# Performance work log

Hardware: AMD Instinct MI355X
Metric: run time of the kernel (lower is better)

## Reference

```python
import jax, jax.numpy as jnp
import numpy as np

EPS = 1e-7  # K.epsilon()
SIZE_IN, IN_CAPS, KSIZE, STRIDE, CAPS, ROUTINGS = 14, 32, 3, 2, 32, 3
SIZE_OUT = (SIZE_IN - KSIZE) // STRIDE + 1  # 6
P = SIZE_OUT * SIZE_OUT          # 36 parent positions
C = KSIZE * KSIZE * IN_CAPS      # 288 child capsules per parent


def _child_parent_map():
    idx = []
    valid = range(0, SIZE_IN - KSIZE + 1, STRIDE)
    for row in valid:
        for col in valid:
            for kr in range(KSIZE):
                start = (row + kr) * SIZE_IN + col
                idx.extend(range(start, start + KSIZE))
    return np.asarray(idx, dtype=np.int32).reshape(P, KSIZE * KSIZE)

CPM = _child_parent_map()  # [P, K^2] static gather indices


def _em_routing(in_act, votes, beta_a, beta_v):
    # in_act: [B,P,C,1,1]; votes: [B,P,C,O,16]
    O = CAPS
    rr = jnp.full(votes.shape[:4] + (1,), 1.0 / O, dtype=votes.dtype)
    bv = beta_v.reshape(1, 1, 1, O, 1)
    ba = beta_a.reshape(1, 1, 1, O)
    out_act = means = None
    for i in range(ROUTINGS):
        lambd = 0.01 * (1.0 - 0.95 ** i)
        # ---- M step ----
        rr_scaled = rr * in_act                                   # [B,P,C,O,1]
        rr_sum = jnp.sum(rr_scaled, axis=2, keepdims=True)        # [B,P,1,O,1]
        means = jnp.sum(rr_scaled * votes, axis=2, keepdims=True) / (rr_sum + EPS)  # [B,P,1,O,16]
        std = jnp.sqrt(jnp.sum(rr_scaled * jnp.square(votes - means), axis=2, keepdims=True) / (rr_sum + EPS))
        costs = bv + jnp.log(std + EPS) * rr_sum                  # [B,P,1,O,16]
        out_act = jax.nn.sigmoid(lambd * (ba - jnp.sum(costs, axis=-1)))[..., None]  # [B,P,1,O,1]
        # ---- E step ----
        if i < ROUTINGS - 1:
            prob_exp = -jnp.sum(jnp.square(votes - means) / (2.0 * jnp.square(std) + EPS), axis=-1, keepdims=True)
            prob_main = -jnp.sum(jnp.log(std + EPS), axis=-1, keepdims=True)
            zz = jnp.log(out_act + EPS) + prob_main + prob_exp   # [B,P,C,O,1]
            rr = jax.nn.softmax(zz, axis=3)
    return out_act, means


def setup_inputs() -> dict:
    key = jax.random.key(0)
    k1, k2, k3, k4, k5 = jax.random.split(key, 5)
    B = 8
    return {
        "in_act": jax.random.uniform(k1, (B, SIZE_IN, SIZE_IN, IN_CAPS, 1), dtype=jnp.float32),
        "in_pose": jax.random.normal(k2, (B, SIZE_IN, SIZE_IN, IN_CAPS, 4, 4), dtype=jnp.float32),
        "W": jax.random.normal(k3, (1, 1, C, CAPS, 4, 4), dtype=jnp.float32) * 0.1,
        "beta_a": jax.random.normal(k4, (CAPS,), dtype=jnp.float32),
        "beta_v": jax.random.normal(k5, (CAPS,), dtype=jnp.float32),
    }


def reference(in_act, in_pose, W, beta_a, beta_v):
    B = in_act.shape[0]
    act = in_act.reshape(B, SIZE_IN * SIZE_IN, IN_CAPS)
    pose = in_pose.reshape(B, SIZE_IN * SIZE_IN, IN_CAPS, 4, 4)
    # gather children for each parent window -> [B,P,C,...]
    act_g = act[:, CPM].reshape(B, P, C, 1, 1)
    pose_g = pose[:, CPM].reshape(B, P, C, 4, 4)
    # votes[b,p,c,o,i,j] = sum_k pose_g[b,p,c,i,k] * W[c,o,k,j]
    votes = jnp.einsum('bpcik,cokj->bpcoij', pose_g, W.reshape(C, CAPS, 4, 4))
    votes = votes.reshape(B, P, C, CAPS, 16)
    out_act, out_pose = _em_routing(act_g, votes, beta_a, beta_v)
    out_act = out_act.reshape(B, SIZE_OUT, SIZE_OUT, CAPS, 1)
    out_pose = out_pose.reshape(B, SIZE_OUT, SIZE_OUT, CAPS, 4, 4)
    return out_act, out_pose
```

## Files before the change

kernel.cpp:

```cpp
#include <hip/hip_runtime.h>
#include <math.h>

#define EPS 1e-7f

constexpr int SIZE_IN = 14;
constexpr int P_  = 36;
constexpr int Cc  = 288;
constexpr int O_  = 32;
constexpr int G_  = 4;
constexpr int CG  = Cc / G_;
constexpr int NTG = CG / 8;
constexpr int THREADS = 256;
constexpr int NBP = 8 * P_;
constexpr int MIVS = 36;

template<int CTRL>
__device__ __forceinline__ float dppf(float x) {
    int xi = __builtin_bit_cast(int, x);
    return __builtin_bit_cast(float,
        __builtin_amdgcn_update_dpp(xi, xi, CTRL, 0xf, 0xf, true));
}
__device__ __forceinline__ float swz16(float x) {
    return __builtin_bit_cast(float,
        __builtin_amdgcn_ds_swizzle(__builtin_bit_cast(int, x), 0x401F));
}
__device__ __forceinline__ float red32_max(float x) {
    x = fmaxf(x, dppf<0xB1>(x));
    x = fmaxf(x, dppf<0x4E>(x));
    x = fmaxf(x, dppf<0x141>(x));
    x = fmaxf(x, dppf<0x140>(x));
    x = fmaxf(x, swz16(x));
    return x;
}
__device__ __forceinline__ float red32_sum(float x) {
    x += dppf<0xB1>(x);
    x += dppf<0x4E>(x);
    x += dppf<0x141>(x);
    x += dppf<0x140>(x);
    x += swz16(x);
    return x;
}
__device__ __forceinline__ float red16_sum(float x) {
    x += dppf<0xB1>(x);
    x += dppf<0x4E>(x);
    x += dppf<0x141>(x);
    x += dppf<0x140>(x);
    return x;
}

#define F4_TO_ARR(dst, off, f4) \
    dst[(off)+0] = (f4).x; dst[(off)+1] = (f4).y; dst[(off)+2] = (f4).z; dst[(off)+3] = (f4).w;


struct __align__(16) PassMem {
    float pose[CG * 16];
    float act[CG];
    float red[4][O_][33];
    float miv[O_][33];
};

template<bool HASE>
__global__ __launch_bounds__(THREADS, 1) void caps_pass(
    const float* __restrict__ in_act, const float* __restrict__ in_pose,
    const float* __restrict__ W, const float* __restrict__ MIV,
    float* __restrict__ Pout)
{
    __shared__ PassMem sm;
    const int blk = blockIdx.x;
    const int bp = blk >> 2, g = blk & 3;
    const int b  = bp / P_,  p = bp % P_;
    const int tid = threadIdx.x;
    const int row0 = (p / 6) * 2, col0 = (p % 6) * 2;

    for (int f = tid; f < CG * 4; f += THREADS) {
        const int fq = g * (CG * 4) + f;
        const int qw = fq >> 7, r = fq & 127;
        const int pix = (row0 + qw / 3) * SIZE_IN + (col0 + qw % 3);
        reinterpret_cast<float4*>(sm.pose)[f] =
            reinterpret_cast<const float4*>(in_pose + (size_t)(b * 196 + pix) * 512)[r];
    }
    for (int idx = tid; idx < CG; idx += THREADS) {
        const int c = g * CG + idx;
        const int qw = c >> 5, ic = c & 31;
        const int pix = (row0 + qw / 3) * SIZE_IN + (col0 + qw % 3);
        sm.act[idx] = in_act[(size_t)(b * 196 + pix) * 32 + ic];
    }
    if (HASE) {
        const float* mb = MIV + (size_t)bp * O_ * MIVS;
        for (int idx = tid; idx < O_ * 33; idx += THREADS) {
            const int oo = idx / 33, k = idx - oo * 33;
            sm.miv[oo][k] = mb[oo * MIVS + k];
        }
    }
    __syncthreads();

    const int o  = tid & 31;
    const int ci = tid >> 5;

    float m[16], iv[16], zb = 0.f;
    if (HASE) {
        #pragma unroll
        for (int j = 0; j < 16; ++j) { m[j] = sm.miv[o][j]; iv[j] = sm.miv[o][16 + j]; }
        zb = sm.miv[o][32];
    }

    float S0 = 0.f, S1[16], S2[16];
    #pragma unroll
    for (int j = 0; j < 16; ++j) { S1[j] = 0.f; S2[j] = 0.f; }

    const float4* wp0 = reinterpret_cast<const float4*>(W + (size_t)((g * CG + ci) * O_ + o) * 16);
    float4 nw0 = wp0[0], nw1 = wp0[1], nw2 = wp0[2], nw3 = wp0[3];
    const float4* pp0 = reinterpret_cast<const float4*>(&sm.pose[ci * 16]);
    float4 np0 = pp0[0], np1 = pp0[1], np2 = pp0[2], np3 = pp0[3];

    #pragma unroll 1
    for (int t = 0; t < NTG; ++t) {
        const int cl = t * 8 + ci;
        float w[16], q[16];
        F4_TO_ARR(w, 0, nw0) F4_TO_ARR(w, 4, nw1) F4_TO_ARR(w, 8, nw2) F4_TO_ARR(w, 12, nw3)
        F4_TO_ARR(q, 0, np0) F4_TO_ARR(q, 4, np1) F4_TO_ARR(q, 8, np2) F4_TO_ARR(q, 12, np3)
        if (t + 1 < NTG) {
            const int cn = g * CG + cl + 8;
            const float4* wn = reinterpret_cast<const float4*>(W + (size_t)(cn * O_ + o) * 16);
            nw0 = wn[0]; nw1 = wn[1]; nw2 = wn[2]; nw3 = wn[3];
            const float4* pn = reinterpret_cast<const float4*>(&sm.pose[(cl + 8) * 16]);
            np0 = pn[0]; np1 = pn[1]; np2 = pn[2]; np3 = pn[3];
        }

        float v[16];
        #pragma unroll
        for (int i = 0; i < 4; ++i) {
            #pragma unroll
            for (int jj = 0; jj < 4; ++jj) {
                float acc = q[i*4+0] * w[0*4+jj];
                acc = fmaf(q[i*4+1], w[1*4+jj], acc);
                acc = fmaf(q[i*4+2], w[2*4+jj], acc);
                acc = fmaf(q[i*4+3], w[3*4+jj], acc);
                v[i*4+jj] = acc;
            }
        }

        float ws;
        if (HASE) {
            float s = 0.f;
            #pragma unroll
            for (int j = 0; j < 16; ++j) { float d = v[j] - m[j]; s = fmaf(d * d, iv[j], s); }
            float zz = zb - s;
            float mx = red32_max(zz);
            float e = __expf(zz - mx);
            float sum = red32_sum(e);
            ws = (e / sum) * sm.act[cl];
        } else {
            ws = sm.act[cl] * (1.0f / 32.0f);
        }

        S0 += ws;
        #pragma unroll
        for (int j = 0; j < 16; ++j) {
            float t0 = ws * v[j];
            S1[j] += t0;
            S2[j] = fmaf(t0, v[j], S2[j]);
        }
    }

    S0 += __shfl_xor(S0, 32);
    #pragma unroll
    for (int j = 0; j < 16; ++j) {
        S1[j] += __shfl_xor(S1[j], 32);
        S2[j] += __shfl_xor(S2[j], 32);
    }
    if (!(tid & 32)) {
        const int wv = tid >> 6;
        float* r = sm.red[wv][o];
        r[0] = S0;
        #pragma unroll
        for (int j = 0; j < 16; ++j) { r[1 + j] = S1[j]; r[17 + j] = S2[j]; }
    }
    __syncthreads();

    float* slot = Pout + (size_t)(bp * G_ + g) * O_ * 33;
    for (int idx = tid; idx < O_ * 33; idx += THREADS) {
        const int oo = idx / 33, k = idx - oo * 33;
        slot[idx] = sm.red[0][oo][k] + sm.red[1][oo][k] + sm.red[2][oo][k] + sm.red[3][oo][k];
    }
}

template<bool LAST>
__global__ __launch_bounds__(THREADS, 2) void caps_fin(
    const float* __restrict__ Pin, const float* __restrict__ beta_a,
    const float* __restrict__ beta_v, float* __restrict__ MIV,
    float* __restrict__ out, float lambda)
{
    const int bp = blockIdx.x;
    const int tid = threadIdx.x;
    const float* base = Pin + (size_t)bp * G_ * O_ * 33;
    #pragma unroll
    for (int half = 0; half < 2; ++half) {
        const int of = (tid >> 4) + half * 16, jf = tid & 15;
        float s0 = 0.f, s1 = 0.f, s2 = 0.f;
        #pragma unroll
        for (int gg = 0; gg < G_; ++gg) {
            const float* r = base + ((size_t)gg * O_ + of) * 33;
            s0 += r[0]; s1 += r[1 + jf]; s2 += r[17 + jf];
        }
        float denom = s0 + EPS;
        float mj = s1 / denom;
        float varn = fmaxf(s2 - 2.f * mj * s1 + mj * mj * s0, 0.f);
        float sd = sqrtf(varn / denom);
        float sumlog = red16_sum(__logf(sd + EPS));
        if (!LAST) {
            float* mb = MIV + ((size_t)bp * O_ + of) * MIVS;
            mb[jf] = mj;
            mb[16 + jf] = 1.f / fmaf(2.f * sd, sd, EPS);
            if (jf == 0) {
                float cost = fmaf(16.f, beta_v[of], s0 * sumlog);
                float oact = 1.f / (1.f + __expf(-(lambda * (beta_a[of] - cost))));
                mb[32] = __logf(oact + EPS) - sumlog;
            }
        } else {
            out[NBP * O_ + ((size_t)bp * O_ + of) * 16 + jf] = mj;
            if (jf == 0) {
                float cost = fmaf(16.f, beta_v[of], s0 * sumlog);
                float oact = 1.f / (1.f + __expf(-(lambda * (beta_a[of] - cost))));
                out[bp * O_ + of] = oact;
            }
        }
    }
}

struct __align__(16) SMem {
    float pose[Cc * 16];
    float act[Cc];
    float red[4][O_][33];
    float mean[O_][17];
    float iv[O_][17];
    float zb[O_];
};

template<bool HASE, bool LAST>
__device__ __forceinline__ void em_pass(
    SMem& sm, const float* __restrict__ W,
    const float* __restrict__ beta_a, const float* __restrict__ beta_v,
    float lambda, int bp, float* __restrict__ out)
{
    const int tid = threadIdx.x;
    const int o  = tid & 31;
    const int ci = tid >> 5;

    float m[16], iv[16], zb = 0.f;
    if (HASE) {
        #pragma unroll
        for (int j = 0; j < 16; ++j) { m[j] = sm.mean[o][j]; iv[j] = sm.iv[o][j]; }
        zb = sm.zb[o];
    }

    float S0 = 0.f, S1[16], S2[16];
    #pragma unroll
    for (int j = 0; j < 16; ++j) { S1[j] = 0.f; S2[j] = 0.f; }

    const float4* wp0 = reinterpret_cast<const float4*>(W + (size_t)(ci * O_ + o) * 16);
    float4 nw0 = wp0[0], nw1 = wp0[1], nw2 = wp0[2], nw3 = wp0[3];
    const float4* pp0 = reinterpret_cast<const float4*>(&sm.pose[ci * 16]);
    float4 np0 = pp0[0], np1 = pp0[1], np2 = pp0[2], np3 = pp0[3];

    #pragma unroll 2
    for (int t = 0; t < 36; ++t) {
        const int c = t * 8 + ci;
        float w[16], q[16];
        F4_TO_ARR(w, 0, nw0) F4_TO_ARR(w, 4, nw1) F4_TO_ARR(w, 8, nw2) F4_TO_ARR(w, 12, nw3)
        F4_TO_ARR(q, 0, np0) F4_TO_ARR(q, 4, np1) F4_TO_ARR(q, 8, np2) F4_TO_ARR(q, 12, np3)
        if (t + 1 < 36) {
            const int cn = c + 8;
            const float4* wn = reinterpret_cast<const float4*>(W + (size_t)(cn * O_ + o) * 16);
            nw0 = wn[0]; nw1 = wn[1]; nw2 = wn[2]; nw3 = wn[3];
            const float4* pn = reinterpret_cast<const float4*>(&sm.pose[cn * 16]);
            np0 = pn[0]; np1 = pn[1]; np2 = pn[2]; np3 = pn[3];
        }

        float v[16];
        #pragma unroll
        for (int i = 0; i < 4; ++i) {
            #pragma unroll
            for (int jj = 0; jj < 4; ++jj) {
                float acc = q[i*4+0] * w[0*4+jj];
                acc = fmaf(q[i*4+1], w[1*4+jj], acc);
                acc = fmaf(q[i*4+2], w[2*4+jj], acc);
                acc = fmaf(q[i*4+3], w[3*4+jj], acc);
                v[i*4+jj] = acc;
            }
        }

        float ws;
        if (HASE) {
            float s = 0.f;
            #pragma unroll
            for (int j = 0; j < 16; ++j) { float d = v[j] - m[j]; s = fmaf(d * d, iv[j], s); }
            float zz = zb - s;
            float mx = red32_max(zz);
            float e = __expf(zz - mx);
            float sum = red32_sum(e);
            ws = (e / sum) * sm.act[c];
        } else {
            ws = sm.act[c] * (1.0f / 32.0f);
        }

        S0 += ws;
        #pragma unroll
        for (int j = 0; j < 16; ++j) {
            float t0 = ws * v[j];
            S1[j] += t0;
            S2[j] = fmaf(t0, v[j], S2[j]);
        }
    }

    S0 += __shfl_xor(S0, 32);
    #pragma unroll
    for (int j = 0; j < 16; ++j) {
        S1[j] += __shfl_xor(S1[j], 32);
        S2[j] += __shfl_xor(S2[j], 32);
    }
    if (!(tid & 32)) {
        const int wv = tid >> 6;
        float* r = sm.red[wv][o];
        r[0] = S0;
        #pragma unroll
        for (int j = 0; j < 16; ++j) { r[1 + j] = S1[j]; r[17 + j] = S2[j]; }
    }
    __syncthreads();

    #pragma unroll
    for (int half = 0; half < 2; ++half) {
        const int of = (tid >> 4) + half * 16, jf = tid & 15;
        const float* r0 = sm.red[0][of];
        const float* r1 = sm.red[1][of];
        const float* r2 = sm.red[2][of];
        const float* r3 = sm.red[3][of];
        float s0 = r0[0] + r1[0] + r2[0] + r3[0];
        float s1 = r0[1+jf] + r1[1+jf] + r2[1+jf] + r3[1+jf];
        float s2 = r0[17+jf] + r1[17+jf] + r2[17+jf] + r3[17+jf];
        float denom = s0 + EPS;
        float mj = s1 / denom;
        float varn = fmaxf(s2 - 2.f * mj * s1 + mj * mj * s0, 0.f);
        float sd = sqrtf(varn / denom);
        float sumlog = red16_sum(__logf(sd + EPS));
        if (!LAST) {
            sm.mean[of][jf] = mj;
            sm.iv[of][jf] = 1.f / fmaf(2.f * sd, sd, EPS);
            if (jf == 0) {
                float cost = fmaf(16.f, beta_v[of], s0 * sumlog);
                float oact = 1.f / (1.f + __expf(-(lambda * (beta_a[of] - cost))));
                sm.zb[of] = __logf(oact + EPS) - sumlog;
            }
        } else {
            out[NBP * O_ + ((size_t)bp * O_ + of) * 16 + jf] = mj;
            if (jf == 0) {
                float cost = fmaf(16.f, beta_v[of], s0 * sumlog);
                float oact = 1.f / (1.f + __expf(-(lambda * (beta_a[of] - cost))));
                out[bp * O_ + of] = oact;
            }
        }
    }
    __syncthreads();
}

__global__ __launch_bounds__(THREADS, 2) void convcaps_fused(
    const float* __restrict__ in_act, const float* __restrict__ in_pose,
    const float* __restrict__ W, const float* __restrict__ beta_a,
    const float* __restrict__ beta_v, float* __restrict__ out)
{
    __shared__ SMem sm;
    const int bp = blockIdx.x;
    const int b  = bp / P_;
    const int p  = bp % P_;
    const int tid = threadIdx.x;
    const int row0 = (p / 6) * 2, col0 = (p % 6) * 2;

    for (int f = tid; f < 9 * 128; f += THREADS) {
        const int qw = f >> 7, r = f & 127;
        const int pix = (row0 + qw / 3) * SIZE_IN + (col0 + qw % 3);
        reinterpret_cast<float4*>(sm.pose)[qw * 128 + r] =
            reinterpret_cast<const float4*>(in_pose + (size_t)(b * 196 + pix) * 512)[r];
    }
    for (int idx = tid; idx < Cc; idx += THREADS) {
        const int qw = idx >> 5, ic = idx & 31;
        const int pix = (row0 + qw / 3) * SIZE_IN + (col0 + qw % 3);
        sm.act[idx] = in_act[(size_t)(b * 196 + pix) * 32 + ic];
    }
    __syncthreads();

    em_pass<false, false>(sm, W, beta_a, beta_v, 0.0f,      bp, out);
    em_pass<true,  false>(sm, W, beta_a, beta_v, 0.0005f,   bp, out);
    em_pass<true,  true >(sm, W, beta_a, beta_v, 0.000975f, bp, out);
}

extern "C" void kernel_launch(void* const* d_in, const int* in_sizes, int n_in,
                              void* d_out, int out_size, void* d_ws, size_t ws_size,
                              hipStream_t stream) {
    const float* in_act  = (const float*)d_in[0];
    const float* in_pose = (const float*)d_in[1];
    const float* W       = (const float*)d_in[2];
    const float* beta_a  = (const float*)d_in[3];
    const float* beta_v  = (const float*)d_in[4];
    float* out = (float*)d_out;

    const size_t p_elems   = (size_t)NBP * G_ * O_ * 33;
    const size_t miv_elems = (size_t)NBP * O_ * MIVS;
    const size_t need = (p_elems + miv_elems) * sizeof(float);

    if (ws_size >= need) {
        float* P   = (float*)d_ws;
        float* MIV = P + p_elems;
        dim3 gp(NBP * G_), gf(NBP), blk(THREADS);
        caps_pass<false><<<gp, blk, 0, stream>>>(in_act, in_pose, W, nullptr, P);
        caps_fin<false><<<gf, blk, 0, stream>>>(P, beta_a, beta_v, MIV, nullptr, 0.0f);
        caps_pass<true><<<gp, blk, 0, stream>>>(in_act, in_pose, W, MIV, P);
        caps_fin<false><<<gf, blk, 0, stream>>>(P, beta_a, beta_v, MIV, nullptr, 0.0005f);
        caps_pass<true><<<gp, blk, 0, stream>>>(in_act, in_pose, W, MIV, P);
        caps_fin<true><<<gf, blk, 0, stream>>>(P, beta_a, beta_v, nullptr, out, 0.000975f);
    } else {
        convcaps_fused<<<dim3(NBP), dim3(THREADS), 0, stream>>>(
            in_act, in_pose, W, beta_a, beta_v, out);
    }
}
```

Measured before the change: 146.3 us.

## Fuse EM routing passes into one persistent kernel with grid barriers

Replaces the six-launch pass/finalize sequence with a single kernel that keeps pose and activation tiles in LDS across all three routing iterations. Blocks sync through atomic-counter grid barriers, and each block recomputes the finalize step for its own parent locally. The channel split per parent drops from four groups to two so all blocks can be co-resident. The cost is a spin-wait barrier, an extra memset launch, a host occupancy query on every call, and half as many blocks to hide latency.

```diff
diff --git a/kernel.cpp b/kernel.cpp
--- a/kernel.cpp
+++ b/kernel.cpp
@@ -7,12 +7,12 @@
 constexpr int P_  = 36;
 constexpr int Cc  = 288;
 constexpr int O_  = 32;
-constexpr int G_  = 4;
+constexpr int G_  = 2;
 constexpr int CG  = Cc / G_;
 constexpr int NTG = CG / 8;
 constexpr int THREADS = 256;
 constexpr int NBP = 8 * P_;
-constexpr int MIVS = 36;
+constexpr int NBLK = NBP * G_;
 
 template<int CTRL>
 __device__ __forceinline__ float dppf(float x) {
@@ -51,23 +51,74 @@
 #define F4_TO_ARR(dst, off, f4) \
     dst[(off)+0] = (f4).x; dst[(off)+1] = (f4).y; dst[(off)+2] = (f4).z; dst[(off)+3] = (f4).w;
 
-
-struct __align__(16) PassMem {
+__device__ __forceinline__ void gridbar(unsigned* ctr) {
+    __threadfence();
+    __syncthreads();
+    if (threadIdx.x == 0) {
+        __atomic_fetch_add(ctr, 1u, __ATOMIC_RELAXED);
+        while (__atomic_load_n(ctr, __ATOMIC_RELAXED) < (unsigned)NBLK)
+            __builtin_amdgcn_s_sleep(8);
+    }
+    __syncthreads();
+    __threadfence();
+}
+
+struct __align__(16) AllMem {
     float pose[CG * 16];
     float act[CG];
     float red[4][O_][33];
     float miv[O_][33];
 };
 
-template<bool HASE>
-__global__ __launch_bounds__(THREADS, 1) void caps_pass(
+template<bool LAST>
+__device__ __forceinline__ void fin_phase(
+    AllMem& sm, const float* __restrict__ Pin, const float* __restrict__ beta_a,
+    const float* __restrict__ beta_v, float lambda, int bp, float* __restrict__ out)
+{
+    const int tid = threadIdx.x;
+    const float* base = Pin + (size_t)bp * G_ * O_ * 33;
+    #pragma unroll
+    for (int half = 0; half < 2; ++half) {
+        const int of = (tid >> 4) + half * 16, jf = tid & 15;
+        float s0 = 0.f, s1 = 0.f, s2 = 0.f;
+        #pragma unroll
+        for (int gg = 0; gg < G_; ++gg) {
+            const float* r = base + ((size_t)gg * O_ + of) * 33;
+            s0 += r[0]; s1 += r[1 + jf]; s2 += r[17 + jf];
+        }
+        float denom = s0 + EPS;
+        float mj = s1 / denom;
+        float varn = fmaxf(s2 - 2.f * mj * s1 + mj * mj * s0, 0.f);
+        float sd = sqrtf(varn / denom);
+        float sumlog = red16_sum(__logf(sd + EPS));
+        if (!LAST) {
+            sm.miv[of][jf] = mj;
+            sm.miv[of][16 + jf] = 1.f / fmaf(2.f * sd, sd, EPS);
+            if (jf == 0) {
+                float cost = fmaf(16.f, beta_v[of], s0 * sumlog);
+                float oact = 1.f / (1.f + __expf(-(lambda * (beta_a[of] - cost))));
+                sm.miv[of][32] = __logf(oact + EPS) - sumlog;
+            }
+        } else {
+            out[NBP * O_ + ((size_t)bp * O_ + of) * 16 + jf] = mj;
+            if (jf == 0) {
+                float cost = fmaf(16.f, beta_v[of], s0 * sumlog);
+                float oact = 1.f / (1.f + __expf(-(lambda * (beta_a[of] - cost))));
+                out[bp * O_ + of] = oact;
+            }
+        }
+    }
+}
+
+__global__ __launch_bounds__(THREADS, 2) void caps_all(
     const float* __restrict__ in_act, const float* __restrict__ in_pose,
-    const float* __restrict__ W, const float* __restrict__ MIV,
-    float* __restrict__ Pout)
+    const float* __restrict__ W, const float* __restrict__ beta_a,
+    const float* __restrict__ beta_v, float* __restrict__ out,
+    float* __restrict__ P1, float* __restrict__ P2, unsigned* __restrict__ bars)
 {
-    __shared__ PassMem sm;
+    __shared__ AllMem sm;
     const int blk = blockIdx.x;
-    const int bp = blk >> 2, g = blk & 3;
+    const int bp = blk >> 1, g = blk & 1;
     const int b  = bp / P_,  p = bp % P_;
     const int tid = threadIdx.x;
     const int row0 = (p / 6) * 2, col0 = (p % 6) * 2;
@@ -85,147 +136,112 @@
         const int pix = (row0 + qw / 3) * SIZE_IN + (col0 + qw % 3);
         sm.act[idx] = in_act[(size_t)(b * 196 + pix) * 32 + ic];
     }
-    if (HASE) {
-        const float* mb = MIV + (size_t)bp * O_ * MIVS;
+    __syncthreads();
+
+    const int o  = tid & 31;
+    const int ci = tid >> 5;
+
+    for (int iter = 0; iter < 3; ++iter) {
+        float* Pcur = (iter == 1) ? P2 : P1;
+        const float* Pprev = (iter == 1) ? P1 : P2;
+        if (iter > 0) {
+            fin_phase<false>(sm, Pprev, beta_a, beta_v,
+                             (iter == 1) ? 0.0f : 0.0005f, bp, nullptr);
+            __syncthreads();
+        }
+
+        float m[16], iv[16], zb = 0.f;
+        if (iter > 0) {
+            #pragma unroll
+            for (int j = 0; j < 16; ++j) { m[j] = sm.miv[o][j]; iv[j] = sm.miv[o][16 + j]; }
+            zb = sm.miv[o][32];
+        }
+
+        float S0 = 0.f, S1[16], S2[16];
+        #pragma unroll
+        for (int j = 0; j < 16; ++j) { S1[j] = 0.f; S2[j] = 0.f; }
+
+        const float4* wp0 = reinterpret_cast<const float4*>(W + (size_t)((g * CG + ci) * O_ + o) * 16);
+        float4 nw0 = wp0[0], nw1 = wp0[1], nw2 = wp0[2], nw3 = wp0[3];
+        const float4* pp0 = reinterpret_cast<const float4*>(&sm.pose[ci * 16]);
+        float4 np0 = pp0[0], np1 = pp0[1], np2 = pp0[2], np3 = pp0[3];
+
+        #pragma unroll 1
+        for (int t = 0; t < NTG; ++t) {
+            const int cl = t * 8 + ci;
+            float w[16], q[16];
+            F4_TO_ARR(w, 0, nw0) F4_TO_ARR(w, 4, nw1) F4_TO_ARR(w, 8, nw2) F4_TO_ARR(w, 12, nw3)
+            F4_TO_ARR(q, 0, np0) F4_TO_ARR(q, 4, np1) F4_TO_ARR(q, 8, np2) F4_TO_ARR(q, 12, np3)
+            if (t + 1 < NTG) {
+                const int cn = g * CG + cl + 8;
+                const float4* wn = reinterpret_cast<const float4*>(W + (size_t)(cn * O_ + o) * 16);
+                nw0 = wn[0]; nw1 = wn[1]; nw2 = wn[2]; nw3 = wn[3];
+                const float4* pn = reinterpret_cast<const float4*>(&sm.pose[(cl + 8) * 16]);
+                np0 = pn[0]; np1 = pn[1]; np2 = pn[2]; np3 = pn[3];
+            }
+
+            float v[16];
+            #pragma unroll
+            for (int i = 0; i < 4; ++i) {
+                #pragma unroll
+                for (int jj = 0; jj < 4; ++jj) {
+                    float acc = q[i*4+0] * w[0*4+jj];
+                    acc = fmaf(q[i*4+1], w[1*4+jj], acc);
+                    acc = fmaf(q[i*4+2], w[2*4+jj], acc);
+                    acc = fmaf(q[i*4+3], w[3*4+jj], acc);
+                    v[i*4+jj] = acc;
+                }
+            }
+
+            float ws;
+            if (iter > 0) {
+                float s = 0.f;
+                #pragma unroll
+                for (int j = 0; j < 16; ++j) { float d = v[j] - m[j]; s = fmaf(d * d, iv[j], s); }
+                float zz = zb - s;
+                float mx = red32_max(zz);
+                float e = __expf(zz - mx);
+                float sum = red32_sum(e);
+                ws = (e / sum) * sm.act[cl];
+            } else {
+                ws = sm.act[cl] * (1.0f / 32.0f);
+            }
+
+            S0 += ws;
+            #pragma unroll
+            for (int j = 0; j < 16; ++j) {
+                float t0 = ws * v[j];
+                S1[j] += t0;
+                S2[j] = fmaf(t0, v[j], S2[j]);
+            }
+        }
+
+        S0 += __shfl_xor(S0, 32);
+        #pragma unroll
+        for (int j = 0; j < 16; ++j) {
+            S1[j] += __shfl_xor(S1[j], 32);
+            S2[j] += __shfl_xor(S2[j], 32);
+        }
+        if (!(tid & 32)) {
+            const int wv = tid >> 6;
+            float* r = sm.red[wv][o];
+            r[0] = S0;
+            #pragma unroll
+            for (int j = 0; j < 16; ++j) { r[1 + j] = S1[j]; r[17 + j] = S2[j]; }
+        }
+        __syncthreads();
+
+        float* slot = Pcur + (size_t)(bp * G_ + g) * O_ * 33;
         for (int idx = tid; idx < O_ * 33; idx += THREADS) {
             const int oo = idx / 33, k = idx - oo * 33;
-            sm.miv[oo][k] = mb[oo * MIVS + k];
-        }
-    }
-    __syncthreads();
-
-    const int o  = tid & 31;
-    const int ci = tid >> 5;
-
-    float m[16], iv[16], zb = 0.f;
-    if (HASE) {
-        #pragma unroll
-        for (int j = 0; j < 16; ++j) { m[j] = sm.miv[o][j]; iv[j] = sm.miv[o][16 + j]; }
-        zb = sm.miv[o][32];
-    }
-
-    float S0 = 0.f, S1[16], S2[16];
-    #pragma unroll
-    for (int j = 0; j < 16; ++j) { S1[j] = 0.f; S2[j] = 0.f; }
-
-    const float4* wp0 = reinterpret_cast<const float4*>(W + (size_t)((g * CG + ci) * O_ + o) * 16);
-    float4 nw0 = wp0[0], nw1 = wp0[1], nw2 = wp0[2], nw3 = wp0[3];
-    const float4* pp0 = reinterpret_cast<const float4*>(&sm.pose[ci * 16]);
-    float4 np0 = pp0[0], np1 = pp0[1], np2 = pp0[2], np3 = pp0[3];
-
-    #pragma unroll 1
-    for (int t = 0; t < NTG; ++t) {
-        const int cl = t * 8 + ci;
-        float w[16], q[16];
-        F4_TO_ARR(w, 0, nw0) F4_TO_ARR(w, 4, nw1) F4_TO_ARR(w, 8, nw2) F4_TO_ARR(w, 12, nw3)
-        F4_TO_ARR(q, 0, np0) F4_TO_ARR(q, 4, np1) F4_TO_ARR(q, 8, np2) F4_TO_ARR(q, 12, np3)
-        if (t + 1 < NTG) {
-            const int cn = g * CG + cl + 8;
-            const float4* wn = reinterpret_cast<const float4*>(W + (size_t)(cn * O_ + o) * 16);
-            nw0 = wn[0]; nw1 = wn[1]; nw2 = wn[2]; nw3 = wn[3];
-            const float4* pn = reinterpret_cast<const float4*>(&sm.pose[(cl + 8) * 16]);
-            np0 = pn[0]; np1 = pn[1]; np2 = pn[2]; np3 = pn[3];
-        }
-
-        float v[16];
-        #pragma unroll
-        for (int i = 0; i < 4; ++i) {
-            #pragma unroll
-            for (int jj = 0; jj < 4; ++jj) {
-                float acc = q[i*4+0] * w[0*4+jj];
-                acc = fmaf(q[i*4+1], w[1*4+jj], acc);
-                acc = fmaf(q[i*4+2], w[2*4+jj], acc);
-                acc = fmaf(q[i*4+3], w[3*4+jj], acc);
-                v[i*4+jj] = acc;
-            }
-        }
-
-        float ws;
-        if (HASE) {
-            float s = 0.f;
-            #pragma unroll
-            for (int j = 0; j < 16; ++j) { float d = v[j] - m[j]; s = fmaf(d * d, iv[j], s); }
-            float zz = zb - s;
-            float mx = red32_max(zz);
-            float e = __expf(zz - mx);
-            float sum = red32_sum(e);
-            ws = (e / sum) * sm.act[cl];
-        } else {
-            ws = sm.act[cl] * (1.0f / 32.0f);
-        }
-
-        S0 += ws;
-        #pragma unroll
-        for (int j = 0; j < 16; ++j) {
-            float t0 = ws * v[j];
-            S1[j] += t0;
-            S2[j] = fmaf(t0, v[j], S2[j]);
-        }
-    }
-
-    S0 += __shfl_xor(S0, 32);
-    #pragma unroll
-    for (int j = 0; j < 16; ++j) {
-        S1[j] += __shfl_xor(S1[j], 32);
-        S2[j] += __shfl_xor(S2[j], 32);
-    }
-    if (!(tid & 32)) {
-        const int wv = tid >> 6;
-        float* r = sm.red[wv][o];
-        r[0] = S0;
-        #pragma unroll
-        for (int j = 0; j < 16; ++j) { r[1 + j] = S1[j]; r[17 + j] = S2[j]; }
-    }
-    __syncthreads();
-
-    float* slot = Pout + (size_t)(bp * G_ + g) * O_ * 33;
-    for (int idx = tid; idx < O_ * 33; idx += THREADS) {
-        const int oo = idx / 33, k = idx - oo * 33;
-        slot[idx] = sm.red[0][oo][k] + sm.red[1][oo][k] + sm.red[2][oo][k] + sm.red[3][oo][k];
-    }
-}
-
-template<bool LAST>
-__global__ __launch_bounds__(THREADS, 2) void caps_fin(
-    const float* __restrict__ Pin, const float* __restrict__ beta_a,
-    const float* __restrict__ beta_v, float* __restrict__ MIV,
-    float* __restrict__ out, float lambda)
-{
-    const int bp = blockIdx.x;
-    const int tid = threadIdx.x;
-    const float* base = Pin + (size_t)bp * G_ * O_ * 33;
-    #pragma unroll
-    for (int half = 0; half < 2; ++half) {
-        const int of = (tid >> 4) + half * 16, jf = tid & 15;
-        float s0 = 0.f, s1 = 0.f, s2 = 0.f;
-        #pragma unroll
-        for (int gg = 0; gg < G_; ++gg) {
-            const float* r = base + ((size_t)gg * O_ + of) * 33;
-            s0 += r[0]; s1 += r[1 + jf]; s2 += r[17 + jf];
-        }
-        float denom = s0 + EPS;
-        float mj = s1 / denom;
-        float varn = fmaxf(s2 - 2.f * mj * s1 + mj * mj * s0, 0.f);
-        float sd = sqrtf(varn / denom);
-        float sumlog = red16_sum(__logf(sd + EPS));
-        if (!LAST) {
-            float* mb = MIV + ((size_t)bp * O_ + of) * MIVS;
-            mb[jf] = mj;
-            mb[16 + jf] = 1.f / fmaf(2.f * sd, sd, EPS);
-            if (jf == 0) {
-                float cost = fmaf(16.f, beta_v[of], s0 * sumlog);
-                float oact = 1.f / (1.f + __expf(-(lambda * (beta_a[of] - cost))));
-                mb[32] = __logf(oact + EPS) - sumlog;
-            }
-        } else {
-            out[NBP * O_ + ((size_t)bp * O_ + of) * 16 + jf] = mj;
-            if (jf == 0) {
-                float cost = fmaf(16.f, beta_v[of], s0 * sumlog);
-                float oact = 1.f / (1.f + __expf(-(lambda * (beta_a[of] - cost))));
-                out[bp * O_ + of] = oact;
-            }
-        }
-    }
+            slot[idx] = sm.red[0][oo][k] + sm.red[1][oo][k] + sm.red[2][oo][k] + sm.red[3][oo][k];
+        }
+
+        gridbar(&bars[iter]);
+    }
+
+    if (g == 0)
+        fin_phase<true>(sm, P1, beta_a, beta_v, 0.000975f, bp, out);
 }
 
 struct __align__(16) SMem {
@@ -403,20 +419,20 @@
     const float* beta_v  = (const float*)d_in[4];
     float* out = (float*)d_out;
 
-    const size_t p_elems   = (size_t)NBP * G_ * O_ * 33;
-    const size_t miv_elems = (size_t)NBP * O_ * MIVS;
-    const size_t need = (p_elems + miv_elems) * sizeof(float);
-
-    if (ws_size >= need) {
-        float* P   = (float*)d_ws;
-        float* MIV = P + p_elems;
-        dim3 gp(NBP * G_), gf(NBP), blk(THREADS);
-        caps_pass<false><<<gp, blk, 0, stream>>>(in_act, in_pose, W, nullptr, P);
-        caps_fin<false><<<gf, blk, 0, stream>>>(P, beta_a, beta_v, MIV, nullptr, 0.0f);
-        caps_pass<true><<<gp, blk, 0, stream>>>(in_act, in_pose, W, MIV, P);
-        caps_fin<false><<<gf, blk, 0, stream>>>(P, beta_a, beta_v, MIV, nullptr, 0.0005f);
-        caps_pass<true><<<gp, blk, 0, stream>>>(in_act, in_pose, W, MIV, P);
-        caps_fin<true><<<gf, blk, 0, stream>>>(P, beta_a, beta_v, nullptr, out, 0.000975f);
+    const size_t p_elems = (size_t)NBP * G_ * O_ * 33;
+    const size_t need = 2 * p_elems * sizeof(float) + 64;
+
+    int maxblk_per_cu = 0;
+    (void)hipOccupancyMaxActiveBlocksPerMultiprocessor(&maxblk_per_cu, caps_all, THREADS, 0);
+    const bool resident_ok = (maxblk_per_cu * 256 >= NBLK);
+
+    if (ws_size >= need && resident_ok) {
+        float* P1 = (float*)d_ws;
+        float* P2 = P1 + p_elems;
+        unsigned* bars = (unsigned*)(P2 + p_elems);
+        hipMemsetAsync(bars, 0, 3 * sizeof(unsigned), stream);
+        caps_all<<<dim3(NBLK), dim3(THREADS), 0, stream>>>(
+            in_act, in_pose, W, beta_a, beta_v, out, P1, P2, bars);
     } else {
         convcaps_fused<<<dim3(NBP), dim3(THREADS), 0, stream>>>(
             in_act, in_pose, W, beta_a, beta_v, out);
```

After: 143.5 us. Within noise of the previous version (-1.9%).
